# Optimization experiments

Hardware: AMD Instinct MI355X
Metric: run time of the kernel (lower is better)

The kernel has to match this reference:

```python
import jax, jax.numpy as jnp
import numpy as np

B, T, D, U = 64, 2048, 256, 256

def setup_inputs() -> dict:
    key = jax.random.key(0)
    ks = jax.random.split(key, 8)
    return {
        "query": jax.random.normal(ks[0], (B, D), dtype=jnp.float32),
        "values": jax.random.normal(ks[1], (B, T, D), dtype=jnp.float32),
        "W1_w": jax.random.normal(ks[2], (D, U), dtype=jnp.float32) * 0.05,
        "W1_b": jnp.zeros((U,), dtype=jnp.float32),
        "W2_w": jax.random.normal(ks[3], (D, U), dtype=jnp.float32) * 0.05,
        "W2_b": jnp.zeros((U,), dtype=jnp.float32),
        "V_w": jax.random.normal(ks[4], (U, 1), dtype=jnp.float32) * 0.05,
        "V_b": jnp.zeros((1,), dtype=jnp.float32),
    }

def reference(query, values, W1_w, W1_b, W2_w, W2_b, V_w, V_b):
    # query: [B, D] -> [B, 1, U]
    q_proj = (query @ W1_w + W1_b)[:, None, :]
    # values: [B, T, D] -> [B, T, U]
    v_proj = jnp.einsum('btd,du->btu', values, W2_w) + W2_b
    # score: [B, T, 1]
    score = jnp.tanh(q_proj + v_proj) @ V_w + V_b
    attention_weights = jax.nn.softmax(score, axis=1)  # over time axis
    context_vector = jnp.sum(attention_weights * values, axis=1)  # [B, D]
    return (context_vector, attention_weights)
```

## Files before the change

### kernel.cpp

```cpp
#include <hip/hip_runtime.h>
#include <hip/hip_fp16.h>

#define B_ 64
#define T_ 2048
#define D_ 256
#define U_ 256
#define BM 64

typedef _Float16 half8 __attribute__((ext_vector_type(8)));
typedef _Float16 half4v __attribute__((ext_vector_type(4)));
typedef float    floatx4 __attribute__((ext_vector_type(4)));

__global__ void qproj_kernel(const float* __restrict__ query,
                             const float* __restrict__ W1_w,
                             const float* __restrict__ W1_b,
                             const float* __restrict__ W2_b,
                             float* __restrict__ qb) {
    __shared__ float qrow[D_];
    const int b = blockIdx.x;
    const int u = threadIdx.x;
    qrow[u] = query[b * D_ + u];
    __syncthreads();
    float acc = W1_b[u] + W2_b[u];
#pragma unroll 8
    for (int d = 0; d < D_; ++d)
        acc += qrow[d] * W1_w[d * U_ + u];
    qb[b * U_ + u] = acc;
}

__global__ void w2t_kernel(const float* __restrict__ W2_w, _Float16* __restrict__ w2t) {
    __shared__ float tile[32][33];
    const int tu = blockIdx.x & 7;
    const int td = blockIdx.x >> 3;
    const int c  = threadIdx.x & 31;
    const int r0 = threadIdx.x >> 5;
#pragma unroll
    for (int i = 0; i < 4; ++i) {
        int r = r0 + i * 8;
        tile[r][c] = W2_w[(td * 32 + r) * U_ + tu * 32 + c];
    }
    __syncthreads();
#pragma unroll
    for (int i = 0; i < 4; ++i) {
        int r = r0 + i * 8;
        w2t[(tu * 32 + r) * D_ + td * 32 + c] = (_Float16)tile[c][r];
    }
}

__launch_bounds__(256, 2)
__global__ void score_kernel(const float* __restrict__ values,
                             const _Float16* __restrict__ w2t,
                             const float* __restrict__ qb,
                             const float* __restrict__ V_w,
                             float* __restrict__ scores) {
    constexpr int LDP = D_ + 8;
    __shared__ _Float16 lds_v[16 * LDP];
    __shared__ float s_part[4][16];

    const int b    = blockIdx.y;
    const int tblk = blockIdx.x;
    const int tid  = threadIdx.x;
    const int wave = tid >> 6;
    const int lane = tid & 63;
    const int n16  = lane & 15;
    const int quad = lane >> 4;
    const int u0   = wave * 64;

    half8 bfrag[4][8];
#pragma unroll
    for (int ut = 0; ut < 4; ++ut) {
        const int u = u0 + ut * 16 + n16;
#pragma unroll
        for (int k = 0; k < 8; ++k)
            bfrag[ut][k] = *(const half8*)(w2t + u * D_ + k * 32 + quad * 8);
    }
    float qbv[4], vwv[4];
#pragma unroll
    for (int ut = 0; ut < 4; ++ut) {
        const int u = u0 + ut * 16 + n16;
        qbv[ut] = qb[b * U_ + u];
        vwv[ut] = V_w[u];
    }

    const float* vbase = values + (size_t)b * T_ * D_ + (size_t)tblk * BM * D_;

    for (int tt = 0; tt < 4; ++tt) {
        const float* src = vbase + tt * 16 * D_;
#pragma unroll
        for (int rep = 0; rep < 4; ++rep) {
            const int f   = tid + rep * 256;
            const int row = f >> 6;
            const int dd  = (f & 63) * 4;
            floatx4 v = *(const floatx4*)(src + row * D_ + dd);
            half4v h;
            h.x = (_Float16)v.x; h.y = (_Float16)v.y;
            h.z = (_Float16)v.z; h.w = (_Float16)v.w;
            *(half4v*)(&lds_v[row * LDP + dd]) = h;
        }
        __syncthreads();

        floatx4 acc[4] = {};
#pragma unroll
        for (int k = 0; k < 8; ++k) {
            half8 a = *(const half8*)(&lds_v[n16 * LDP + k * 32 + quad * 8]);
#pragma unroll
            for (int ut = 0; ut < 4; ++ut)
                acc[ut] = __builtin_amdgcn_mfma_f32_16x16x32_f16(a, bfrag[ut][k], acc[ut], 0, 0, 0);
        }

        float part[4];
#pragma unroll
        for (int r = 0; r < 4; ++r) {
            float s = 0.f;
#pragma unroll
            for (int ut = 0; ut < 4; ++ut) {
                float x  = acc[ut][r] + qbv[ut];
                float e  = __expf(2.f * x);
                float th = 1.f - __fdividef(2.f, e + 1.f);
                s += th * vwv[ut];
            }
            part[r] = s;
        }
#pragma unroll
        for (int m = 1; m < 16; m <<= 1)
#pragma unroll
            for (int r = 0; r < 4; ++r)
                part[r] += __shfl_xor(part[r], m, 16);
        if (n16 == 0)
#pragma unroll
            for (int r = 0; r < 4; ++r)
                s_part[wave][quad * 4 + r] = part[r];
        __syncthreads();
        if (tid < 16) {
            float s = s_part[0][tid] + s_part[1][tid] + s_part[2][tid] + s_part[3][tid];
            scores[b * T_ + tblk * BM + tt * 16 + tid] = s;
        }
        __syncthreads();
    }
}

__global__ void softmax_kernel(const float* __restrict__ scores, float* __restrict__ attn) {
    const int b   = blockIdx.x;
    const int tid = threadIdx.x;
    const float* s = scores + b * T_;
    float v[8];
    float mx = -1e30f;
#pragma unroll
    for (int i = 0; i < 8; ++i) {
        v[i] = s[tid + i * 256];
        mx = fmaxf(mx, v[i]);
    }
    for (int m = 32; m >= 1; m >>= 1) mx = fmaxf(mx, __shfl_xor(mx, m, 64));
    __shared__ float wmax[4], wsum[4];
    const int wave = tid >> 6, lane = tid & 63;
    if (lane == 0) wmax[wave] = mx;
    __syncthreads();
    mx = fmaxf(fmaxf(wmax[0], wmax[1]), fmaxf(wmax[2], wmax[3]));
    float sum = 0.f;
#pragma unroll
    for (int i = 0; i < 8; ++i) { v[i] = __expf(v[i] - mx); sum += v[i]; }
    for (int m = 32; m >= 1; m >>= 1) sum += __shfl_xor(sum, m, 64);
    if (lane == 0) wsum[wave] = sum;
    __syncthreads();
    sum = wsum[0] + wsum[1] + wsum[2] + wsum[3];
    const float inv = 1.f / sum;
#pragma unroll
    for (int i = 0; i < 8; ++i) attn[b * T_ + tid + i * 256] = v[i] * inv;
}

__global__ void context_kernel(const float* __restrict__ values,
                               const float* __restrict__ attn,
                               float* __restrict__ ctx) {
    __shared__ float w[256];
    const int b     = blockIdx.y;
    const int chunk = blockIdx.x;
    const int tid   = threadIdx.x;
    w[tid] = attn[b * T_ + chunk * 256 + tid];
    __syncthreads();
    const int r = tid >> 6;
    const int c = tid & 63;
    const float* vb = values + (size_t)b * T_ * D_ + (size_t)chunk * 256 * D_;
    floatx4 acc = {0.f, 0.f, 0.f, 0.f};
#pragma unroll 4
    for (int i = 0; i < 64; ++i) {
        const int t = i * 4 + r;
        floatx4 vv = *(const floatx4*)(vb + t * D_ + c * 4);
        acc += vv * w[t];
    }
    atomicAdd(&ctx[b * D_ + c * 4 + 0], acc.x);
    atomicAdd(&ctx[b * D_ + c * 4 + 1], acc.y);
    atomicAdd(&ctx[b * D_ + c * 4 + 2], acc.z);
    atomicAdd(&ctx[b * D_ + c * 4 + 3], acc.w);
}

extern "C" void kernel_launch(void* const* d_in, const int* in_sizes, int n_in,
                              void* d_out, int out_size, void* d_ws, size_t ws_size,
                              hipStream_t stream) {
    const float* query  = (const float*)d_in[0];
    const float* values = (const float*)d_in[1];
    const float* W1_w   = (const float*)d_in[2];
    const float* W1_b   = (const float*)d_in[3];
    const float* W2_w   = (const float*)d_in[4];
    const float* W2_b   = (const float*)d_in[5];
    const float* V_w    = (const float*)d_in[6];

    float* out  = (float*)d_out;
    float* ctx  = out;
    float* attn = out + B_ * D_;

    char* ws = (char*)d_ws;
    float*     qb     = (float*)ws;
    _Float16*  w2t    = (_Float16*)(ws + 65536);
    float*     scores = (float*)(ws + 65536 + 131072);

    hipMemsetAsync(ctx, 0, B_ * D_ * sizeof(float), stream);
    qproj_kernel  <<<dim3(B_),        dim3(256), 0, stream>>>(query, W1_w, W1_b, W2_b, qb);
    w2t_kernel    <<<dim3(64),        dim3(256), 0, stream>>>(W2_w, w2t);
    score_kernel  <<<dim3(T_/BM, B_), dim3(256), 0, stream>>>(values, w2t, qb, V_w, scores);
    softmax_kernel<<<dim3(B_),        dim3(256), 0, stream>>>(scores, attn);
    context_kernel<<<dim3(8, B_),     dim3(256), 0, stream>>>(values, attn, ctx);
}
```

Measured before the change: 274.5 us.

## Fuse score, online softmax, and context into one kernel with async LDS staging

Merges the score, softmax and context kernels into a single pass that computes scores and, in the same pass, an online-softmax weighted context per 256-step chunk. A small finalize kernel then rescales and combines the chunk partials and writes the attention weights. Values are staged into swizzled fp32 LDS with double-buffered global_load_lds and converted to fp16 at MFMA time. This removes the second full read of the 134MB values tensor and the atomics, but cuts the grid to 512 blocks and adds serial per-tile syncs on a 16-thread softmax step.

```diff
diff --git a/kernel.cpp b/kernel.cpp
--- a/kernel.cpp
+++ b/kernel.cpp
@@ -1,15 +1,20 @@
 #include <hip/hip_runtime.h>
 #include <hip/hip_fp16.h>
+#include <stdint.h>
 
 #define B_ 64
 #define T_ 2048
 #define D_ 256
 #define U_ 256
-#define BM 64
-
-typedef _Float16 half8 __attribute__((ext_vector_type(8)));
-typedef _Float16 half4v __attribute__((ext_vector_type(4)));
+#define BT 256
+#define NT (BT / 16)
+#define TC (T_ / BT)
+
+typedef _Float16 half8  __attribute__((ext_vector_type(8)));
 typedef float    floatx4 __attribute__((ext_vector_type(4)));
+
+typedef const __attribute__((address_space(1))) void cg_void;
+typedef __attribute__((address_space(3))) void       ls_void;
 
 __global__ void qproj_kernel(const float* __restrict__ query,
                              const float* __restrict__ W1_w,
@@ -48,23 +53,26 @@
 }
 
 __launch_bounds__(256, 2)
-__global__ void score_kernel(const float* __restrict__ values,
-                             const _Float16* __restrict__ w2t,
-                             const float* __restrict__ qb,
-                             const float* __restrict__ V_w,
-                             float* __restrict__ scores) {
-    constexpr int LDP = D_ + 8;
-    __shared__ _Float16 lds_v[16 * LDP];
+__global__ void score_ctx_kernel(const float* __restrict__ values,
+                                 const _Float16* __restrict__ w2t,
+                                 const float* __restrict__ qb,
+                                 const float* __restrict__ V_w,
+                                 float* __restrict__ scores,
+                                 float* __restrict__ pctx,
+                                 float* __restrict__ pml) {
+    __shared__ __align__(16) float buf[2][16 * D_];
     __shared__ float s_part[4][16];
-
-    const int b    = blockIdx.y;
-    const int tblk = blockIdx.x;
-    const int tid  = threadIdx.x;
-    const int wave = tid >> 6;
-    const int lane = tid & 63;
-    const int n16  = lane & 15;
-    const int quad = lane >> 4;
-    const int u0   = wave * 64;
+    __shared__ float wbuf[16];
+    __shared__ float alphabuf;
+
+    const int b     = blockIdx.y;
+    const int chunk = blockIdx.x;
+    const int tid   = threadIdx.x;
+    const int wave  = tid >> 6;
+    const int lane  = tid & 63;
+    const int n16   = lane & 15;
+    const int quad  = lane >> 4;
+    const int u0    = wave * 64;
 
     half8 bfrag[4][8];
 #pragma unroll
@@ -82,27 +90,43 @@
         vwv[ut] = V_w[u];
     }
 
-    const float* vbase = values + (size_t)b * T_ * D_ + (size_t)tblk * BM * D_;
-
-    for (int tt = 0; tt < 4; ++tt) {
-        const float* src = vbase + tt * 16 * D_;
-#pragma unroll
-        for (int rep = 0; rep < 4; ++rep) {
-            const int f   = tid + rep * 256;
-            const int row = f >> 6;
-            const int dd  = (f & 63) * 4;
-            floatx4 v = *(const floatx4*)(src + row * D_ + dd);
-            half4v h;
-            h.x = (_Float16)v.x; h.y = (_Float16)v.y;
-            h.z = (_Float16)v.z; h.w = (_Float16)v.w;
-            *(half4v*)(&lds_v[row * LDP + dd]) = h;
-        }
+    const float* vbase = values + (size_t)b * T_ * D_ + (size_t)chunk * BT * D_;
+
+    float c     = 0.f;
+    float m_run = -1e30f;
+    float l_run = 0.f;
+
+    auto stage = [&](int tile, int bi) {
+        const float* src = vbase + tile * 16 * D_;
+#pragma unroll
+        for (int i = 0; i < 4; ++i) {
+            const int r = i * 4 + wave;
+            const float* g = src + r * D_ + ((lane ^ (r & 7)) << 2);
+            float* l = &buf[bi][r * D_];
+            __builtin_amdgcn_global_load_lds((cg_void*)g, (ls_void*)l, 16, 0, 0);
+        }
+    };
+
+    stage(0, 0);
+
+    for (int tile = 0; tile < NT; ++tile) {
+        const int cur = tile & 1;
         __syncthreads();
+        if (tile + 1 < NT) stage(tile + 1, cur ^ 1);
 
         floatx4 acc[4] = {};
+        const float* rowbase = &buf[cur][n16 * D_];
+        const int swz = n16 & 7;
 #pragma unroll
         for (int k = 0; k < 8; ++k) {
-            half8 a = *(const half8*)(&lds_v[n16 * LDP + k * 32 + quad * 8]);
+            const int c0 = k * 8 + quad * 2;
+            floatx4 q0 = *(const floatx4*)(rowbase + (((c0    ) ^ swz) << 2));
+            floatx4 q1 = *(const floatx4*)(rowbase + (((c0 + 1) ^ swz) << 2));
+            half8 a;
+            a[0] = (_Float16)q0.x; a[1] = (_Float16)q0.y;
+            a[2] = (_Float16)q0.z; a[3] = (_Float16)q0.w;
+            a[4] = (_Float16)q1.x; a[5] = (_Float16)q1.y;
+            a[6] = (_Float16)q1.z; a[7] = (_Float16)q1.w;
 #pragma unroll
             for (int ut = 0; ut < 4; ++ut)
                 acc[ut] = __builtin_amdgcn_mfma_f32_16x16x32_f16(a, bfrag[ut][k], acc[ut], 0, 0, 0);
@@ -131,66 +155,70 @@
             for (int r = 0; r < 4; ++r)
                 s_part[wave][quad * 4 + r] = part[r];
         __syncthreads();
+
         if (tid < 16) {
             float s = s_part[0][tid] + s_part[1][tid] + s_part[2][tid] + s_part[3][tid];
-            scores[b * T_ + tblk * BM + tt * 16 + tid] = s;
+            scores[b * T_ + chunk * BT + tile * 16 + tid] = s;
+            float mt = s;
+#pragma unroll
+            for (int m = 1; m < 16; m <<= 1) mt = fmaxf(mt, __shfl_xor(mt, m, 16));
+            const float m_new = fmaxf(m_run, mt);
+            const float alpha = __expf(m_run - m_new);
+            const float w     = __expf(s - m_new);
+            float ls = w;
+#pragma unroll
+            for (int m = 1; m < 16; m <<= 1) ls += __shfl_xor(ls, m, 16);
+            l_run = l_run * alpha + ls;
+            m_run = m_new;
+            wbuf[tid] = w;
+            if (tid == 0) alphabuf = alpha;
         }
         __syncthreads();
-    }
-}
-
-__global__ void softmax_kernel(const float* __restrict__ scores, float* __restrict__ attn) {
-    const int b   = blockIdx.x;
-    const int tid = threadIdx.x;
-    const float* s = scores + b * T_;
-    float v[8];
-    float mx = -1e30f;
-#pragma unroll
-    for (int i = 0; i < 8; ++i) {
-        v[i] = s[tid + i * 256];
-        mx = fmaxf(mx, v[i]);
-    }
-    for (int m = 32; m >= 1; m >>= 1) mx = fmaxf(mx, __shfl_xor(mx, m, 64));
-    __shared__ float wmax[4], wsum[4];
-    const int wave = tid >> 6, lane = tid & 63;
-    if (lane == 0) wmax[wave] = mx;
-    __syncthreads();
-    mx = fmaxf(fmaxf(wmax[0], wmax[1]), fmaxf(wmax[2], wmax[3]));
-    float sum = 0.f;
-#pragma unroll
-    for (int i = 0; i < 8; ++i) { v[i] = __expf(v[i] - mx); sum += v[i]; }
-    for (int m = 32; m >= 1; m >>= 1) sum += __shfl_xor(sum, m, 64);
-    if (lane == 0) wsum[wave] = sum;
-    __syncthreads();
-    sum = wsum[0] + wsum[1] + wsum[2] + wsum[3];
-    const float inv = 1.f / sum;
-#pragma unroll
-    for (int i = 0; i < 8; ++i) attn[b * T_ + tid + i * 256] = v[i] * inv;
-}
-
-__global__ void context_kernel(const float* __restrict__ values,
-                               const float* __restrict__ attn,
-                               float* __restrict__ ctx) {
-    __shared__ float w[256];
-    const int b     = blockIdx.y;
-    const int chunk = blockIdx.x;
-    const int tid   = threadIdx.x;
-    w[tid] = attn[b * T_ + chunk * 256 + tid];
-    __syncthreads();
-    const int r = tid >> 6;
-    const int c = tid & 63;
-    const float* vb = values + (size_t)b * T_ * D_ + (size_t)chunk * 256 * D_;
-    floatx4 acc = {0.f, 0.f, 0.f, 0.f};
-#pragma unroll 4
-    for (int i = 0; i < 64; ++i) {
-        const int t = i * 4 + r;
-        floatx4 vv = *(const floatx4*)(vb + t * D_ + c * 4);
-        acc += vv * w[t];
-    }
-    atomicAdd(&ctx[b * D_ + c * 4 + 0], acc.x);
-    atomicAdd(&ctx[b * D_ + c * 4 + 1], acc.y);
-    atomicAdd(&ctx[b * D_ + c * 4 + 2], acc.z);
-    atomicAdd(&ctx[b * D_ + c * 4 + 3], acc.w);
+
+        const float alpha = alphabuf;
+        c *= alpha;
+        const int ccx = tid >> 2, lo = tid & 3;
+#pragma unroll
+        for (int t = 0; t < 16; ++t) {
+            float v = buf[cur][t * D_ + (((ccx) ^ (t & 7)) << 2) + lo];
+            c += wbuf[t] * v;
+        }
+    }
+
+    pctx[(b * TC + chunk) * D_ + tid] = c;
+    if (tid == 0) {
+        pml[(b * TC + chunk) * 2 + 0] = m_run;
+        pml[(b * TC + chunk) * 2 + 1] = l_run;
+    }
+}
+
+__global__ void finalize_kernel(const float* __restrict__ pctx,
+                                const float* __restrict__ pml,
+                                const float* __restrict__ scores,
+                                float* __restrict__ ctx,
+                                float* __restrict__ attn) {
+    const int b = blockIdx.x, tid = threadIdx.x;
+    float m[TC], l[TC], e[TC];
+    float M = -1e30f;
+#pragma unroll
+    for (int i = 0; i < TC; ++i) {
+        m[i] = pml[(b * TC + i) * 2 + 0];
+        l[i] = pml[(b * TC + i) * 2 + 1];
+        M = fmaxf(M, m[i]);
+    }
+    float L = 0.f;
+#pragma unroll
+    for (int i = 0; i < TC; ++i) { e[i] = __expf(m[i] - M); L += l[i] * e[i]; }
+    float s = 0.f;
+#pragma unroll
+    for (int i = 0; i < TC; ++i) s += pctx[(b * TC + i) * D_ + tid] * e[i];
+    const float invL = 1.f / L;
+    ctx[b * D_ + tid] = s * invL;
+#pragma unroll
+    for (int j = 0; j < T_ / 256; ++j) {
+        const int t = j * 256 + tid;
+        attn[b * T_ + t] = __expf(scores[b * T_ + t] - M) * invL;
+    }
 }
 
 extern "C" void kernel_launch(void* const* d_in, const int* in_sizes, int n_in,
@@ -209,14 +237,14 @@
     float* attn = out + B_ * D_;
 
     char* ws = (char*)d_ws;
-    float*     qb     = (float*)ws;
-    _Float16*  w2t    = (_Float16*)(ws + 65536);
-    float*     scores = (float*)(ws + 65536 + 131072);
-
-    hipMemsetAsync(ctx, 0, B_ * D_ * sizeof(float), stream);
-    qproj_kernel  <<<dim3(B_),        dim3(256), 0, stream>>>(query, W1_w, W1_b, W2_b, qb);
-    w2t_kernel    <<<dim3(64),        dim3(256), 0, stream>>>(W2_w, w2t);
-    score_kernel  <<<dim3(T_/BM, B_), dim3(256), 0, stream>>>(values, w2t, qb, V_w, scores);
-    softmax_kernel<<<dim3(B_),        dim3(256), 0, stream>>>(scores, attn);
-    context_kernel<<<dim3(8, B_),     dim3(256), 0, stream>>>(values, attn, ctx);
-}
+    float*    qb     = (float*)ws;
+    _Float16* w2t    = (_Float16*)(ws + (64 << 10));
+    float*    scores = (float*)(ws + (192 << 10));
+    float*    pctx   = (float*)(ws + (704 << 10));
+    float*    pml    = (float*)(ws + (1216 << 10));
+
+    qproj_kernel    <<<dim3(B_),      dim3(256), 0, stream>>>(query, W1_w, W1_b, W2_b, qb);
+    w2t_kernel      <<<dim3(64),      dim3(256), 0, stream>>>(W2_w, w2t);
+    score_ctx_kernel<<<dim3(TC, B_),  dim3(256), 0, stream>>>(values, w2t, qb, V_w, scores, pctx, pml);
+    finalize_kernel <<<dim3(B_),      dim3(256), 0, stream>>>(pctx, pml, scores, ctx, attn);
+}
```

Measured after the change: 241.6 us. -12.0%, faster.
